# Optimization experiments

Hardware: AMD Instinct MI355X
Metric: run time of the kernel (lower is better)

## Reference

```python
import jax, jax.numpy as jnp
import numpy as np

B, S, D = 4, 2048, 1024
E = 8            # num_experts
H = 2 * D        # int(4*D*(1/top_k)) with top_k=2, scaling_factor='auto'


def setup_inputs() -> dict:
    key = jax.random.key(0)
    ks = jax.random.split(key, 8)
    sd = 1.0 / np.sqrt(D)
    sh = 1.0 / np.sqrt(H)
    return {
        "x": jax.random.normal(ks[0], (B, S, D), dtype=jnp.float32),
        "top_k": 2,
        "Wg": jax.random.uniform(ks[1], (D, E), jnp.float32, -sd, sd),
        "bg": jax.random.uniform(ks[2], (E,), jnp.float32, -sd, sd),
        "W1": jax.random.uniform(ks[3], (E, D, H), jnp.float32, -sd, sd),
        "b1": jax.random.uniform(ks[4], (E, H), jnp.float32, -sd, sd),
        "W2": jax.random.uniform(ks[5], (E, H, D), jnp.float32, -sh, sh),
        "b2": jax.random.uniform(ks[6], (E, D), jnp.float32, -sh, sh),
    }


def reference(x, top_k, Wg, bg, W1, b1, W2, b2):
    b, s, d = x.shape
    e = W1.shape[0]
    T = b * s
    xt = x.reshape(T, d)                                   # [T, D]
    gate_logits = xt @ Wg + bg                             # [T, E]
    gate_probas = jax.nn.softmax(gate_logits, axis=-1)
    topk_p, topk_i = jax.lax.top_k(gate_probas, top_k)     # [T, K]
    topk_p = topk_p / jnp.sum(topk_p, axis=-1, keepdims=True)
    # combine weights per expert: zero for unselected experts
    w = jnp.zeros((T, e), dtype=x.dtype).at[jnp.arange(T)[:, None], topk_i].add(topk_p)  # [T, E]
    # dense grouped FFN over experts; unselected experts are zero-weighted,
    # so the weighted combine matches the original gather-MLP-scatter math
    h = jax.nn.gelu(jnp.einsum('td,edh->teh', xt, W1) + b1, approximate=True)  # [T, E, H]
    y = jnp.einsum('teh,ehd->ted', h, W2) + b2             # [T, E, D]
    out = jnp.einsum('te,ted->td', w, y)                   # [T, D]
    return out.reshape(b, s, d)
```

## Files before the change

### kernel.cpp

```cpp
#include <hip/hip_runtime.h>

typedef unsigned short u16;
typedef short v8s __attribute__((ext_vector_type(8)));
typedef float v4f __attribute__((ext_vector_type(4)));

constexpr int Tn = 8192;
constexpr int Dd = 1024;
constexpr int Hh = 2048;
constexpr int Ee = 8;
constexpr int NB = 32;
constexpr int MAXP = 17;

static __device__ __forceinline__ u16 f2bf(float v) {
  unsigned u = __float_as_uint(v);
  unsigned r = (u + 0x7fffu + ((u >> 16) & 1u)) >> 16;
  return (u16)r;
}

static __device__ __forceinline__ float bf2f(u16 v) {
  return __uint_as_float(((unsigned)v) << 16);
}

static __device__ __forceinline__ void gload_lds16(const u16* g, u16* l) {
  __builtin_amdgcn_global_load_lds(
      (const __attribute__((address_space(1))) unsigned int*)g,
      (__attribute__((address_space(3))) unsigned int*)l, 16, 0, 0);
}

__global__ __launch_bounds__(512) void transpose_cvt_kernel(
    const float* __restrict__ W1, u16* __restrict__ w1t,
    const float* __restrict__ W2, u16* __restrict__ w2t) {
  __shared__ float tile[64][65];
  int b = blockIdx.x;
  const float* in;
  u16* out;
  int R, C, cx, cy, e;
  if (b < 4096) {
    e = b >> 9;
    int t = b & 511;
    R = Dd; C = Hh; cx = t & 31; cy = t >> 5;
    in = W1; out = w1t;
  } else {
    int bb = b - 4096;
    e = bb >> 9;
    int t = bb & 511;
    R = Hh; C = Dd; cx = t & 15; cy = t >> 4;
    in = W2; out = w2t;
  }
  const float* ip = in + (size_t)e * Dd * Hh;
  u16* op = out + (size_t)e * Dd * Hh;
  int c0 = cx * 64, r0 = cy * 64;
  int tx = threadIdx.x, ty = threadIdx.y;
  for (int i = ty; i < 64; i += 8)
    tile[i][tx] = ip[(size_t)(r0 + i) * C + c0 + tx];
  __syncthreads();
  for (int i = ty; i < 64; i += 8)
    op[(size_t)(c0 + i) * R + r0 + tx] = f2bf(tile[tx][i]);
}

__global__ __launch_bounds__(256) void gating_kernel(
    const float* __restrict__ x, const float* __restrict__ Wg, const float* __restrict__ bg,
    int* __restrict__ topki, float* __restrict__ topkw, u16* __restrict__ xb) {
  int lane = threadIdx.x & 63;
  int t = blockIdx.x * 4 + (threadIdx.x >> 6);
  const float4* xr = reinterpret_cast<const float4*>(x + (size_t)t * Dd);
  float acc[8] = {0.f, 0.f, 0.f, 0.f, 0.f, 0.f, 0.f, 0.f};
#pragma unroll
  for (int it = 0; it < 4; ++it) {
    float4 xv = xr[it * 64 + lane];
    int r = it * 256 + lane * 4;
    ushort4 o;
    o.x = f2bf(xv.x); o.y = f2bf(xv.y); o.z = f2bf(xv.z); o.w = f2bf(xv.w);
    *reinterpret_cast<ushort4*>(xb + (size_t)t * Dd + r) = o;
    const float4* wr = reinterpret_cast<const float4*>(Wg + (size_t)r * 8);
    float xs[4] = {xv.x, xv.y, xv.z, xv.w};
#pragma unroll
    for (int q = 0; q < 4; ++q) {
      float4 a = wr[q * 2], b = wr[q * 2 + 1];
      acc[0] += xs[q] * a.x; acc[1] += xs[q] * a.y; acc[2] += xs[q] * a.z; acc[3] += xs[q] * a.w;
      acc[4] += xs[q] * b.x; acc[5] += xs[q] * b.y; acc[6] += xs[q] * b.z; acc[7] += xs[q] * b.w;
    }
  }
#pragma unroll
  for (int e = 0; e < 8; ++e) {
#pragma unroll
    for (int off = 32; off > 0; off >>= 1) acc[e] += __shfl_xor(acc[e], off, 64);
  }
  if (lane == 0) {
    float l[8];
    float mx = -1e30f;
#pragma unroll
    for (int e = 0; e < 8; ++e) { l[e] = acc[e] + bg[e]; mx = fmaxf(mx, l[e]); }
    int i0 = 0;
#pragma unroll
    for (int e = 1; e < 8; ++e) if (l[e] > l[i0]) i0 = e;
    int i1 = (i0 == 0) ? 1 : 0;
#pragma unroll
    for (int e = 0; e < 8; ++e) if (e != i0 && l[e] > l[i1]) i1 = e;
    float e0 = __expf(l[i0] - mx), e1 = __expf(l[i1] - mx);
    float inv = 1.0f / (e0 + e1);
    topki[2 * t] = i0; topki[2 * t + 1] = i1;
    topkw[2 * t] = e0 * inv; topkw[2 * t + 1] = e1 * inv;
  }
}

__global__ __launch_bounds__(256) void hist_kernel(const int* __restrict__ topki,
                                                   int* __restrict__ blockcnt) {
  __shared__ int bins[8];
  int tid = threadIdx.x, b = blockIdx.x;
  if (tid < 8) bins[tid] = 0;
  __syncthreads();
  atomicAdd(&bins[topki[b * 512 + tid]], 1);
  atomicAdd(&bins[topki[b * 512 + 256 + tid]], 1);
  __syncthreads();
  if (tid < 8) blockcnt[b * 8 + tid] = bins[tid];
}

__global__ void prefix_kernel(const int* __restrict__ blockcnt, int* __restrict__ offs,
                              int* __restrict__ blockstart,
                              int* __restrict__ panelE, int* __restrict__ panelB,
                              int* __restrict__ nPanels) {
  __shared__ int tmp[8][NB];
  __shared__ int tot[8];
  int tid = threadIdx.x;
  if (tid < 8) {
    int s = 0;
    for (int b = 0; b < NB; ++b) { tmp[tid][b] = s; s += blockcnt[b * 8 + tid]; }
    tot[tid] = s;
  }
  __syncthreads();
  if (tid == 0) {
    int o = 0;
    for (int e = 0; e < 8; ++e) { offs[e] = o; o += tot[e]; }
    offs[8] = o;
    int np = 0;
    for (int e = 0; e < 8; ++e) {
      for (int m0 = 0; m0 < tot[e]; m0 += 128) {
        panelE[np] = e;
        panelB[np] = offs[e] + m0;
        ++np;
      }
    }
    *nPanels = np;
  }
  __syncthreads();
  if (tid < 8)
    for (int b = 0; b < NB; ++b) blockstart[b * 8 + tid] = offs[tid] + tmp[tid][b];
}

__global__ __launch_bounds__(256) void scatter_kernel(
    const int* __restrict__ topki, const int* __restrict__ blockstart,
    int* __restrict__ rows, int* __restrict__ slotmap) {
  __shared__ int lbins[8];
  int tid = threadIdx.x, b = blockIdx.x;
  if (tid < 8) lbins[tid] = blockstart[b * 8 + tid];
  __syncthreads();
#pragma unroll
  for (int j = 0; j < 2; ++j) {
    int idx = b * 512 + j * 256 + tid;
    int e = topki[idx];
    int slot = atomicAdd(&lbins[e], 1);
    rows[slot] = idx >> 1;
    slotmap[idx] = slot;
  }
}


__global__ __launch_bounds__(256, 2) void gemm1_kernel(
    const u16* __restrict__ xb, const u16* __restrict__ w1t, const float* __restrict__ b1,
    const int* __restrict__ offs, const int* __restrict__ rows,
    const int* __restrict__ panelE, const int* __restrict__ panelB,
    const int* __restrict__ nPanels, u16* __restrict__ hbuf) {
  const int bid = blockIdx.x;
  const int xcd = bid & 7;
  const int q = bid >> 3;
  const int n = q & 15;
  const int pi = (q >> 4) * 8 + xcd;
  if (pi >= *nPanels) return;
  const int e = panelE[pi];
  const int sbase = panelB[pi];
  const int lim = offs[e + 1];
  const int n0 = n * 128;

  __shared__ u16 As[128 * 64];
  __shared__ u16 Bs[128 * 64];

  const int tid = threadIdx.x;
  const int lane = tid & 63;
  const int wid = tid >> 6;
  const int wm = (wid >> 1) * 64;
  const int wn = (wid & 1) * 64;
  const int l16 = lane & 15;
  const int quad = lane >> 4;
  const int swz8 = (l16 & 7) * 8;

  const u16* aga[4];
  const u16* bga[4];
  u16* alds[4];
  u16* blds[4];
  const int lr = lane >> 3;
  const int g = (lane & 7) ^ (lr & 7);
  const int kcol = g * 8;
#pragma unroll
  for (int j = 0; j < 4; ++j) {
    int chunk = wid * 4 + j;
    int rowl = chunk * 8 + lr;
    int slot = sbase + rowl;
    if (slot >= lim) slot = sbase;
    aga[j] = xb + (size_t)rows[slot] * Dd + kcol;
    bga[j] = w1t + ((size_t)e * Hh + n0 + rowl) * Dd + kcol;
    alds[j] = As + chunk * 512;
    blds[j] = Bs + chunk * 512;
  }

  v4f acc[4][4];
#pragma unroll
  for (int i = 0; i < 4; ++i)
#pragma unroll
    for (int j = 0; j < 4; ++j) acc[i][j] = {0.f, 0.f, 0.f, 0.f};

  int rowAoff[4], rowBoff[4];
#pragma unroll
  for (int t_ = 0; t_ < 4; ++t_) {
    rowAoff[t_] = (wm + t_ * 16 + l16) * 64;
    rowBoff[t_] = (wn + t_ * 16 + l16) * 64;
  }

  for (int k0 = 0; k0 < Dd; k0 += 64) {
    __syncthreads();
#pragma unroll
    for (int j = 0; j < 4; ++j) gload_lds16(aga[j] + k0, alds[j]);
#pragma unroll
    for (int j = 0; j < 4; ++j) gload_lds16(bga[j] + k0, blds[j]);
    __syncthreads();

#pragma unroll
    for (int s = 0; s < 2; ++s) {
      int coff = ((s * 4 + quad) * 8) ^ swz8;
      v8s a[4], b[4];
#pragma unroll
      for (int mt = 0; mt < 4; ++mt)
        a[mt] = *reinterpret_cast<const v8s*>(&As[rowAoff[mt] + coff]);
#pragma unroll
      for (int nt = 0; nt < 4; ++nt)
        b[nt] = *reinterpret_cast<const v8s*>(&Bs[rowBoff[nt] + coff]);
#pragma unroll
      for (int mt = 0; mt < 4; ++mt)
#pragma unroll
        for (int nt = 0; nt < 4; ++nt)
          acc[mt][nt] = __builtin_amdgcn_mfma_f32_16x16x32_bf16(a[mt], b[nt], acc[mt][nt], 0, 0, 0);
    }
  }

  float b1v[4];
  int ng[4];
#pragma unroll
  for (int nt = 0; nt < 4; ++nt) {
    ng[nt] = n0 + wn + nt * 16 + l16;
    b1v[nt] = b1[(size_t)e * Hh + ng[nt]];
  }
#pragma unroll
  for (int mt = 0; mt < 4; ++mt) {
#pragma unroll
    for (int i = 0; i < 4; ++i) {
      int m = wm + mt * 16 + quad * 4 + i;
      if (sbase + m < lim) {
        size_t rowbase = (size_t)(sbase + m) * Hh;
#pragma unroll
        for (int nt = 0; nt < 4; ++nt) {
          float v = acc[mt][nt][i] + b1v[nt];
          float s = 1.0f / (1.0f + __expf(-1.5957691216057308f * (v + 0.044715f * v * v * v)));
          hbuf[rowbase + ng[nt]] = f2bf(v * s);
        }
      }
    }
  }
}

__global__ __launch_bounds__(256, 2) void gemm2_kernel(
    const u16* __restrict__ hbuf, const u16* __restrict__ w2t, const float* __restrict__ b2,
    const int* __restrict__ offs,
    const int* __restrict__ panelE, const int* __restrict__ panelB,
    const int* __restrict__ nPanels, u16* __restrict__ ybuf) {
  const int bid = blockIdx.x;
  const int xcd = bid & 7;
  const int q = bid >> 3;
  const int n = q & 7;
  const int pi = (q >> 3) * 8 + xcd;
  if (pi >= *nPanels) return;
  const int e = panelE[pi];
  const int sbase = panelB[pi];
  const int lim = offs[e + 1];
  const int n0 = n * 128;

  __shared__ u16 As[128 * 64];
  __shared__ u16 Bs[128 * 64];

  const int tid = threadIdx.x;
  const int lane = tid & 63;
  const int wid = tid >> 6;
  const int wm = (wid >> 1) * 64;
  const int wn = (wid & 1) * 64;
  const int l16 = lane & 15;
  const int quad = lane >> 4;
  const int swz8 = (l16 & 7) * 8;

  const u16* aga[4];
  const u16* bga[4];
  u16* alds[4];
  u16* blds[4];
  const int lr = lane >> 3;
  const int g = (lane & 7) ^ (lr & 7);
  const int kcol = g * 8;
#pragma unroll
  for (int j = 0; j < 4; ++j) {
    int chunk = wid * 4 + j;
    int rowl = chunk * 8 + lr;
    int slot = sbase + rowl;
    if (slot >= lim) slot = sbase;
    aga[j] = hbuf + (size_t)slot * Hh + kcol;
    bga[j] = w2t + ((size_t)e * Dd + n0 + rowl) * Hh + kcol;
    alds[j] = As + chunk * 512;
    blds[j] = Bs + chunk * 512;
  }

  v4f acc[4][4];
#pragma unroll
  for (int i = 0; i < 4; ++i)
#pragma unroll
    for (int j = 0; j < 4; ++j) acc[i][j] = {0.f, 0.f, 0.f, 0.f};

  int rowAoff[4], rowBoff[4];
#pragma unroll
  for (int t_ = 0; t_ < 4; ++t_) {
    rowAoff[t_] = (wm + t_ * 16 + l16) * 64;
    rowBoff[t_] = (wn + t_ * 16 + l16) * 64;
  }

  for (int k0 = 0; k0 < Hh; k0 += 64) {
    __syncthreads();
#pragma unroll
    for (int j = 0; j < 4; ++j) gload_lds16(aga[j] + k0, alds[j]);
#pragma unroll
    for (int j = 0; j < 4; ++j) gload_lds16(bga[j] + k0, blds[j]);
    __syncthreads();

#pragma unroll
    for (int s = 0; s < 2; ++s) {
      int coff = ((s * 4 + quad) * 8) ^ swz8;
      v8s a[4], b[4];
#pragma unroll
      for (int mt = 0; mt < 4; ++mt)
        a[mt] = *reinterpret_cast<const v8s*>(&As[rowAoff[mt] + coff]);
#pragma unroll
      for (int nt = 0; nt < 4; ++nt)
        b[nt] = *reinterpret_cast<const v8s*>(&Bs[rowBoff[nt] + coff]);
#pragma unroll
      for (int mt = 0; mt < 4; ++mt)
#pragma unroll
        for (int nt = 0; nt < 4; ++nt)
          acc[mt][nt] = __builtin_amdgcn_mfma_f32_16x16x32_bf16(a[mt], b[nt], acc[mt][nt], 0, 0, 0);
    }
  }

  float b2v[4];
  int ng[4];
#pragma unroll
  for (int nt = 0; nt < 4; ++nt) {
    ng[nt] = n0 + wn + nt * 16 + l16;
    b2v[nt] = b2[(size_t)e * Dd + ng[nt]];
  }
#pragma unroll
  for (int mt = 0; mt < 4; ++mt) {
#pragma unroll
    for (int i = 0; i < 4; ++i) {
      int m = wm + mt * 16 + quad * 4 + i;
      if (sbase + m < lim) {
        size_t rowbase = (size_t)(sbase + m) * Dd;
#pragma unroll
        for (int nt = 0; nt < 4; ++nt)
          ybuf[rowbase + ng[nt]] = f2bf(acc[mt][nt][i] + b2v[nt]);
      }
    }
  }
}

__global__ __launch_bounds__(256) void combine_kernel(
    const u16* __restrict__ ybuf, const int* __restrict__ slotmap,
    const float* __restrict__ topkw, float* __restrict__ out) {
  int idx = blockIdx.x * 256 + threadIdx.x;
  int t = idx >> 7;
  int d0 = (idx & 127) * 8;
  int s0 = slotmap[2 * t], s1 = slotmap[2 * t + 1];
  float w0 = topkw[2 * t], w1 = topkw[2 * t + 1];
  uint4 ya = *reinterpret_cast<const uint4*>(ybuf + (size_t)s0 * Dd + d0);
  uint4 yb = *reinterpret_cast<const uint4*>(ybuf + (size_t)s1 * Dd + d0);
  float r[8];
  const unsigned* pa = &ya.x;
  const unsigned* pb = &yb.x;
#pragma unroll
  for (int j = 0; j < 4; ++j) {
    unsigned a = pa[j], b = pb[j];
    r[2 * j]     = w0 * bf2f((u16)(a & 0xffff)) + w1 * bf2f((u16)(b & 0xffff));
    r[2 * j + 1] = w0 * bf2f((u16)(a >> 16))    + w1 * bf2f((u16)(b >> 16));
  }
  float4* op = reinterpret_cast<float4*>(out + (size_t)t * Dd + d0);
  op[0] = make_float4(r[0], r[1], r[2], r[3]);
  op[1] = make_float4(r[4], r[5], r[6], r[7]);
}

extern "C" void kernel_launch(void* const* d_in, const int* in_sizes, int n_in,
                              void* d_out, int out_size, void* d_ws, size_t ws_size,
                              hipStream_t stream) {
  const float* x  = (const float*)d_in[0];
  const float* Wg = (const float*)d_in[2];
  const float* bg = (const float*)d_in[3];
  const float* W1 = (const float*)d_in[4];
  const float* b1 = (const float*)d_in[5];
  const float* W2 = (const float*)d_in[6];
  const float* b2 = (const float*)d_in[7];
  float* out = (float*)d_out;

  char* p = (char*)d_ws;
  auto take = [&](size_t bytes) {
    char* q = p;
    p += (bytes + 255) & ~(size_t)255;
    return q;
  };
  int*   offs       = (int*)take(64);
  int*   blockcnt   = (int*)take((size_t)NB * 8 * sizeof(int));
  int*   blockstart = (int*)take((size_t)NB * 8 * sizeof(int));
  int*   panelE     = (int*)take(1024);
  int*   panelB     = (int*)take(1024);
  int*   nPanels    = (int*)take(256);
  int*   topki      = (int*)take((size_t)Tn * 2 * sizeof(int));
  float* topkw      = (float*)take((size_t)Tn * 2 * sizeof(float));
  int*   rows       = (int*)take((size_t)Tn * 2 * sizeof(int));
  int*   slotmap    = (int*)take((size_t)Tn * 2 * sizeof(int));
  u16*   xb         = (u16*)take((size_t)Tn * Dd * 2);
  u16*   w1t        = (u16*)take((size_t)Ee * Dd * Hh * 2);
  u16*   w2t        = (u16*)take((size_t)Ee * Dd * Hh * 2);
  u16*   hbuf       = (u16*)take((size_t)Tn * 2 * Hh * 2);
  u16*   ybuf       = (u16*)take((size_t)Tn * 2 * Dd * 2);

  transpose_cvt_kernel<<<8192, dim3(64, 8), 0, stream>>>(W1, w1t, W2, w2t);
  gating_kernel<<<Tn / 4, 256, 0, stream>>>(x, Wg, bg, topki, topkw, xb);
  hist_kernel<<<NB, 256, 0, stream>>>(topki, blockcnt);
  prefix_kernel<<<1, 64, 0, stream>>>(blockcnt, offs, blockstart, panelE, panelB, nPanels);
  scatter_kernel<<<NB, 256, 0, stream>>>(topki, blockstart, rows, slotmap);
  gemm1_kernel<<<8 * 16 * MAXP, 256, 0, stream>>>(xb, w1t, b1, offs, rows,
                                                  panelE, panelB, nPanels, hbuf);
  gemm2_kernel<<<8 * 8 * MAXP, 256, 0, stream>>>(hbuf, w2t, b2, offs,
                                                 panelE, panelB, nPanels, ybuf);
  combine_kernel<<<(Tn * Dd / 8) / 256, 256, 0, stream>>>(ybuf, slotmap, topkw, out);
}
```

Measured before the change: 446.7 us.

## Vectorize weight transpose and permute hidden columns for packed hbuf stores

Rewrites the weight transpose/convert kernel to use float4 global loads and 8-wide bf16 stores with 256 threads per block. It also changes the GEMM1 epilogue so each lane writes four bf16 hidden values as one 8-byte store instead of four scattered 2-byte stores. That store pattern permutes hbuf columns inside each 64-wide group, so the W2 transpose applies the matching permutation along H to keep GEMM2 correct. The goals are fewer, wider memory transactions in both kernels. The cost is a strided LDS read pattern in the transpose and a hidden coupling between the GEMM1 tile layout and the W2 preprocessing.

After: 428.6 us. 1.04x faster.

```diff
diff --git a/kernel.cpp b/kernel.cpp
--- a/kernel.cpp
+++ b/kernel.cpp
@@ -3,6 +3,8 @@
 typedef unsigned short u16;
 typedef short v8s __attribute__((ext_vector_type(8)));
 typedef float v4f __attribute__((ext_vector_type(4)));
+typedef u16 u16x8 __attribute__((ext_vector_type(8)));
+typedef u16 u16x4 __attribute__((ext_vector_type(4)));
 
 constexpr int Tn = 8192;
 constexpr int Dd = 1024;
@@ -27,15 +29,17 @@
       (__attribute__((address_space(3))) unsigned int*)l, 16, 0, 0);
 }
 
-__global__ __launch_bounds__(512) void transpose_cvt_kernel(
+
+__global__ __launch_bounds__(256) void transpose_cvt_kernel(
     const float* __restrict__ W1, u16* __restrict__ w1t,
     const float* __restrict__ W2, u16* __restrict__ w2t) {
   __shared__ float tile[64][65];
   int b = blockIdx.x;
+  bool isW1 = b < 4096;
   const float* in;
   u16* out;
   int R, C, cx, cy, e;
-  if (b < 4096) {
+  if (isW1) {
     e = b >> 9;
     int t = b & 511;
     R = Dd; C = Hh; cx = t & 31; cy = t >> 5;
@@ -50,12 +54,35 @@
   const float* ip = in + (size_t)e * Dd * Hh;
   u16* op = out + (size_t)e * Dd * Hh;
   int c0 = cx * 64, r0 = cy * 64;
-  int tx = threadIdx.x, ty = threadIdx.y;
-  for (int i = ty; i < 64; i += 8)
-    tile[i][tx] = ip[(size_t)(r0 + i) * C + c0 + tx];
-  __syncthreads();
-  for (int i = ty; i < 64; i += 8)
-    op[(size_t)(c0 + i) * R + r0 + tx] = f2bf(tile[tx][i]);
+  int tid = threadIdx.x;
+
+#pragma unroll
+  for (int k = 0; k < 4; ++k) {
+    int f = k * 256 + tid;
+    int r = f >> 4, c4 = (f & 15) * 4;
+    float4 v = *reinterpret_cast<const float4*>(ip + (size_t)(r0 + r) * C + c0 + c4);
+    tile[r][c4] = v.x; tile[r][c4 + 1] = v.y; tile[r][c4 + 2] = v.z; tile[r][c4 + 3] = v.w;
+  }
+  __syncthreads();
+
+  int j = tid & 7;
+#pragma unroll
+  for (int rr = 0; rr < 2; ++rr) {
+    int oc = (tid >> 3) + rr * 32;
+    u16x8 o;
+    if (isW1) {
+#pragma unroll
+      for (int q = 0; q < 8; ++q) o[q] = f2bf(tile[j * 8 + q][oc]);
+    } else {
+#pragma unroll
+      for (int q = 0; q < 8; ++q) {
+        int p = j * 8 + q;
+        int src = (p & 3) * 16 + (p >> 2);
+        o[q] = f2bf(tile[src][oc]);
+      }
+    }
+    *reinterpret_cast<u16x8*>(op + (size_t)(c0 + oc) * R + r0 + j * 8) = o;
+  }
 }
 
 __global__ __launch_bounds__(256) void gating_kernel(
@@ -253,25 +280,23 @@
   }
 
   float b1v[4];
-  int ng[4];
-#pragma unroll
-  for (int nt = 0; nt < 4; ++nt) {
-    ng[nt] = n0 + wn + nt * 16 + l16;
-    b1v[nt] = b1[(size_t)e * Hh + ng[nt]];
-  }
+  const int ngbase = n0 + wn;
+#pragma unroll
+  for (int nt = 0; nt < 4; ++nt) b1v[nt] = b1[(size_t)e * Hh + ngbase + nt * 16 + l16];
 #pragma unroll
   for (int mt = 0; mt < 4; ++mt) {
 #pragma unroll
     for (int i = 0; i < 4; ++i) {
       int m = wm + mt * 16 + quad * 4 + i;
       if (sbase + m < lim) {
-        size_t rowbase = (size_t)(sbase + m) * Hh;
+        u16x4 o;
 #pragma unroll
         for (int nt = 0; nt < 4; ++nt) {
           float v = acc[mt][nt][i] + b1v[nt];
           float s = 1.0f / (1.0f + __expf(-1.5957691216057308f * (v + 0.044715f * v * v * v)));
-          hbuf[rowbase + ng[nt]] = f2bf(v * s);
+          o[nt] = f2bf(v * s);
         }
+        *reinterpret_cast<u16x4*>(hbuf + (size_t)(sbase + m) * Hh + ngbase + l16 * 4) = o;
       }
     }
   }
@@ -443,7 +468,7 @@
   u16*   hbuf       = (u16*)take((size_t)Tn * 2 * Hh * 2);
   u16*   ybuf       = (u16*)take((size_t)Tn * 2 * Dd * 2);
 
-  transpose_cvt_kernel<<<8192, dim3(64, 8), 0, stream>>>(W1, w1t, W2, w2t);
+  transpose_cvt_kernel<<<8192, 256, 0, stream>>>(W1, w1t, W2, w2t);
   gating_kernel<<<Tn / 4, 256, 0, stream>>>(x, Wg, bg, topki, topkw, xb);
   hist_kernel<<<NB, 256, 0, stream>>>(topki, blockcnt);
   prefix_kernel<<<1, 64, 0, stream>>>(blockcnt, offs, blockstart, panelE, panelB, nPanels);
```
